# Performance work log

Measured on AMD Instinct MI355X. Metric: run time of the kernel, lower is better.

Reference implementation:

```python
import jax, jax.numpy as jnp
import numpy as np

HEADS = 8
DIM_HEAD = 64
SCALE = DIM_HEAD ** -0.5


def setup_inputs() -> dict:
    key = jax.random.key(0)
    ks = jax.random.split(key, 6)
    b, n, t, d, cond_dim, hidden = 2, 8, 1024, 512, 512, HEADS * DIM_HEAD
    return {
        "x": jax.random.normal(ks[0], (b * n, t, d), dtype=jnp.float32),
        "label_emb_mm": jax.random.normal(ks[1], (b, n, cond_dim), dtype=jnp.float32),
        "Wqkv": jax.random.normal(ks[2], (d, 3 * hidden), dtype=jnp.float32) * (d ** -0.5),
        "Wk": jax.random.normal(ks[3], (cond_dim, hidden), dtype=jnp.float32) * (cond_dim ** -0.5),
        "Wv": jax.random.normal(ks[4], (cond_dim, hidden), dtype=jnp.float32) * (cond_dim ** -0.5),
        "Wout": jax.random.normal(ks[5], (hidden, d), dtype=jnp.float32) * (hidden ** -0.5),
        "b": 2,
    }


def reference(x, label_emb_mm, Wqkv, Wk, Wv, Wout, b):
    bn, t, d = x.shape
    n = bn // b
    h, dh = HEADS, DIM_HEAD
    xb = x.reshape(b, n, t, d)
    # fused QKV projection: (b, n, t, 3*h*dh)
    qkv = xb @ Wqkv
    q, k, v = jnp.split(qkv, 3, axis=-1)

    def to_heads(z):  # (b, n, t, h*dh) -> (b, n, h, t, dh)
        return z.reshape(b, n, t, h, dh).transpose(0, 1, 3, 2, 4)

    q, k, v = to_heads(q), to_heads(k), to_heads(v)
    # per-frame conditioning K/V: one extra token per frame
    ek = (label_emb_mm @ Wk).reshape(b, n, 1, h, dh).transpose(0, 1, 3, 2, 4)
    ev = (label_emb_mm @ Wv).reshape(b, n, 1, h, dh).transpose(0, 1, 3, 2, 4)
    k = jnp.concatenate([ek, k], axis=-2)  # (b, n, h, 1+t, dh)
    v = jnp.concatenate([ev, v], axis=-2)
    q = q * SCALE
    sim = jnp.einsum("bnhid,bnhjd->bnhij", q, k)
    attn = jax.nn.softmax(sim, axis=-1)
    out = jnp.einsum("bnhij,bnhjd->bnhid", attn, v)
    out = out.transpose(0, 1, 3, 2, 4).reshape(b, n, t, h * dh)
    out = out @ Wout
    return out.reshape(b * n, t, d)
```

## Files before the change

kernel.cpp:

```cpp
#include <hip/hip_runtime.h>
#include <stdint.h>

typedef unsigned short u16;
typedef __bf16 bf16x8 __attribute__((ext_vector_type(8)));
typedef float f32x4 __attribute__((ext_vector_type(4)));
typedef float f32x16 __attribute__((ext_vector_type(16)));

__device__ __forceinline__ u16 f2bf(float f) {
  uint32_t u = __builtin_bit_cast(uint32_t, f);
  u += 0x7FFFu + ((u >> 16) & 1u);
  return (u16)(u >> 16);
}
__device__ __forceinline__ float bf2f(u16 v) {
  return __builtin_bit_cast(float, ((uint32_t)v) << 16);
}

#if __has_builtin(__builtin_amdgcn_exp2f)
__device__ __forceinline__ float exp2_fast(float x) { return __builtin_amdgcn_exp2f(x); }
#else
__device__ __forceinline__ float exp2_fast(float x) { return exp2f(x); }
#endif

__device__ __forceinline__ void gload_lds16(const u16* g, u16* l) {
  __builtin_amdgcn_global_load_lds(
      (const __attribute__((address_space(1))) uint32_t*)g,
      (__attribute__((address_space(3))) uint32_t*)l, 16, 0, 0);
}

__device__ __forceinline__ uint32_t cvtpk(float lo, float hi) {
  uint32_t r;
  asm("v_cvt_pk_bf16_f32 %0, %1, %2" : "=v"(r) : "v"(lo), "v"(hi));
  return r;
}
__device__ __forceinline__ void plswap(uint32_t& a, uint32_t& b) {
  asm volatile("v_permlane32_swap_b32 %0, %1" : "+v"(a), "+v"(b));
}

__global__ __launch_bounds__(256) void prep_kernel(
    const float* __restrict__ x, const float* __restrict__ Wqkv,
    const float* __restrict__ Wout, const float* __restrict__ label,
    const float* __restrict__ Wk, const float* __restrict__ Wv,
    u16* __restrict__ xb, u16* __restrict__ WqkvT, u16* __restrict__ WoutT,
    u16* __restrict__ ek, u16* __restrict__ ev, float qscale) {
  const int b = blockIdx.x;
  if (b < 4096) {
    int i = (b * 256 + threadIdx.x) * 8;
    float4 a = *(const float4*)(x + i);
    float4 c = *(const float4*)(x + i + 4);
    union { u16 u[8]; uint4 v; } r;
    r.u[0] = f2bf(a.x); r.u[1] = f2bf(a.y); r.u[2] = f2bf(a.z); r.u[3] = f2bf(a.w);
    r.u[4] = f2bf(c.x); r.u[5] = f2bf(c.y); r.u[6] = f2bf(c.z); r.u[7] = f2bf(c.w);
    *(uint4*)(xb + i) = r.v;
  } else if (b < 7168) {
    int id = (b - 4096) * 256 + threadIdx.x;
    int k = id & 511, nn = id >> 9;
    float v = Wqkv[(size_t)k * 1536 + nn];
    if (nn < 512) v *= qscale;
    WqkvT[id] = f2bf(v);
  } else if (b < 8192) {
    int id = (b - 7168) * 256 + threadIdx.x;
    int k = id & 511, nn = id >> 9;
    WoutT[id] = f2bf(Wout[(size_t)k * 512 + nn]);
  } else {
    __shared__ float sdata[256];
    const int bb = b - 8192;
    const int chunk = bb & 7, row = (bb >> 3) & 15;
    const float* W = (bb & 128) ? Wv : Wk;
    u16* o = (bb & 128) ? ev : ek;
    const int tid = threadIdx.x;
    const int col = chunk * 64 + (tid & 63);
    const int ks = tid >> 6;
    const float* lr = label + row * 512 + ks * 128;
    const float* wp = W + (size_t)(ks * 128) * 512 + col;
    float acc = 0.f;
#pragma unroll 8
    for (int i = 0; i < 128; ++i)
      acc = fmaf(lr[i], wp[(size_t)i * 512], acc);
    sdata[tid] = acc;
    __syncthreads();
    if (tid < 64) {
      float t = sdata[tid] + sdata[tid + 64] + sdata[tid + 128] + sdata[tid + 192];
      o[row * 512 + chunk * 64 + tid] = f2bf(t);
    }
  }
}

template <int MODE>
__global__ __launch_bounds__(512, 2) void gemm_bt_kernel(
    const u16* __restrict__ A, const u16* __restrict__ B,
    u16* __restrict__ OQ, u16* __restrict__ OKb, u16* __restrict__ OVT,
    float* __restrict__ OF, int K, int N) {
  constexpr int BN = (MODE == 0) ? 192 : 128;
  constexpr int NI = BN / 64;
  constexpr int NRB = BN / 64;
  constexpr int NBY = (MODE == 0) ? 8 : 4;
  constexpr int VM = 4 + NRB;

  __shared__ __align__(16) u16 As[2][256 * 64];
  __shared__ __align__(16) u16 Bs[2][BN * 64];

  const int tid = threadIdx.x;
  const int w = tid >> 6, lane = tid & 63;
  const int l15 = lane & 15, lg = lane >> 4;
  const int wr = w >> 2, wc = w & 3;

  const int q8 = gridDim.x >> 3;
  const int wg = (blockIdx.x & 7) * q8 + (blockIdx.x >> 3);
  const int bx = wg / NBY, by = wg % NBY;

  const int srow = tid >> 3, schunk = tid & 7;
  const u16* Ag = A + (size_t)(bx * 256 + srow) * K + ((schunk ^ (srow & 7)) * 8);
  const u16* Bg = B + (size_t)(by * BN + srow) * K + ((schunk ^ (srow & 7)) * 8);

  int aoff[8][2], boff[NI][2];
#pragma unroll
  for (int mi = 0; mi < 8; ++mi)
#pragma unroll
    for (int ks = 0; ks < 2; ++ks) {
      const int row = wr * 128 + mi * 16 + l15;
      aoff[mi][ks] = row * 64 + (((ks * 4 + lg) ^ (row & 7)) * 8);
    }
#pragma unroll
  for (int ni = 0; ni < NI; ++ni)
#pragma unroll
    for (int ks = 0; ks < 2; ++ks) {
      const int row = wc * (BN / 4) + ni * 16 + l15;
      boff[ni][ks] = row * 64 + (((ks * 4 + lg) ^ (row & 7)) * 8);
    }

  f32x4 acc[8][NI] = {};

  const int nt = K >> 6;
#define STAGE(buf, k0)                                                       \
  {                                                                          \
    _Pragma("unroll") for (int ra = 0; ra < 4; ++ra)                         \
        gload_lds16(Ag + (k0) + (size_t)(ra * 64) * K,                       \
                    &As[buf][(ra * 64 + w * 8) * 64]);                       \
    _Pragma("unroll") for (int rb = 0; rb < NRB; ++rb)                       \
        gload_lds16(Bg + (k0) + (size_t)(rb * 64) * K,                       \
                    &Bs[buf][(rb * 64 + w * 8) * 64]);                       \
  }
#define COMPUTE(cb)                                                          \
  {                                                                          \
    const u16* Ab = &As[cb][0];                                              \
    const u16* Bb = &Bs[cb][0];                                              \
    _Pragma("unroll") for (int ks = 0; ks < 2; ++ks) {                       \
      bf16x8 a[8], b[NI];                                                    \
      _Pragma("unroll") for (int mi = 0; mi < 8; ++mi)                       \
          a[mi] = *(const bf16x8*)&Ab[aoff[mi][ks]];                         \
      _Pragma("unroll") for (int ni = 0; ni < NI; ++ni)                      \
          b[ni] = *(const bf16x8*)&Bb[boff[ni][ks]];                         \
      __builtin_amdgcn_s_setprio(1);                                         \
      _Pragma("unroll") for (int mi = 0; mi < 8; ++mi)                       \
          _Pragma("unroll") for (int ni = 0; ni < NI; ++ni)                  \
              acc[mi][ni] = __builtin_amdgcn_mfma_f32_16x16x32_bf16(          \
                  a[mi], b[ni], acc[mi][ni], 0, 0, 0);                       \
      __builtin_amdgcn_s_setprio(0);                                         \
    }                                                                        \
  }

  STAGE(0, 0);
  STAGE(1, 64);

  for (int t = 0; t < nt - 1; ++t) {
    if constexpr (VM == 7)
      asm volatile("s_waitcnt vmcnt(7)" ::: "memory");
    else
      asm volatile("s_waitcnt vmcnt(6)" ::: "memory");
    __builtin_amdgcn_s_barrier();
    __builtin_amdgcn_sched_barrier(0);
    COMPUTE(t & 1);
    if (t + 2 < nt) {
      __builtin_amdgcn_s_barrier();
      __builtin_amdgcn_sched_barrier(0);
      STAGE(t & 1, (t + 2) * 64);
    }
  }
  asm volatile("s_waitcnt vmcnt(0)" ::: "memory");
  __builtin_amdgcn_s_barrier();
  __builtin_amdgcn_sched_barrier(0);
  COMPUTE((nt - 1) & 1);
#undef STAGE
#undef COMPUTE

  const int row0 = bx * 256 + wr * 128 + lg * 4;
  if constexpr (MODE == 1) {
#pragma unroll
    for (int mi = 0; mi < 8; ++mi)
#pragma unroll
      for (int ni = 0; ni < NI; ++ni) {
        int col = by * BN + wc * (BN / 4) + ni * 16 + l15;
#pragma unroll
        for (int r = 0; r < 4; ++r)
          OF[(size_t)(row0 + mi * 16 + r) * N + col] = acc[mi][ni][r];
      }
  } else {
#pragma unroll
    for (int mi = 0; mi < 8; ++mi)
#pragma unroll
      for (int ni = 0; ni < NI; ++ni) {
        const int gcol = by * BN + wc * (BN / 4) + ni * 16 + l15;
        const int sect = gcol >> 9;
        const int colL = gcol & 511;
        if (sect < 2) {
          u16* O = sect ? OKb : OQ;
#pragma unroll
          for (int r = 0; r < 4; ++r)
            O[(size_t)(row0 + mi * 16 + r) * 512 + colL] = f2bf(acc[mi][ni][r]);
        } else {
          int h = colL >> 6, dh = colL & 63;
          int rr = row0 + mi * 16;
          int bn = rr >> 10, t0 = rr & 1023;
          ushort4 pk;
          pk.x = f2bf(acc[mi][ni][0]);
          pk.y = f2bf(acc[mi][ni][1]);
          pk.z = f2bf(acc[mi][ni][2]);
          pk.w = f2bf(acc[mi][ni][3]);
          *(ushort4*)&OVT[(size_t)((bn * 8 + h) * 64 + dh) * 1024 + t0] = pk;
        }
      }
  }
}

__global__ __launch_bounds__(256, 2) void attn_kernel(
    const u16* __restrict__ Qb, const u16* __restrict__ Kb, const u16* __restrict__ VTb,
    const u16* __restrict__ ekb, const u16* __restrict__ evb, u16* __restrict__ Ob) {
  __shared__ __align__(16) u16 Kl[64 * 64];
  __shared__ __align__(16) u16 Vl[64 * 64];

  const int tid = threadIdx.x;
  const int w = tid >> 6, lane = tid & 63;
  const int l31 = lane & 31, hi = lane >> 5;
  const int lb = (blockIdx.x & 7) * 64 + (blockIdx.x >> 3);
  const int head = lb >> 2, qt = lb & 3;
  const int bn = head >> 3, h = head & 7;
  const int q0 = qt * 256 + w * 64;

  const int sr = tid >> 3, sj = tid & 7;
  const int sdst = (sj ^ (sr & 7)) * 8;
  const u16* KgA = Kb + (size_t)(bn * 1024 + sr) * 512 + h * 64 + sj * 8;
  const u16* VgA = VTb + (size_t)(head * 64 + sr) * 1024 + sj * 8;
  u16* KlD = &Kl[sr * 64 + sdst];
  u16* VlD = &Vl[sr * 64 + sdst];

  uint4 kp0, kp1, vp0, vp1;
  {
    kp0 = *(const uint4*)(KgA);
    kp1 = *(const uint4*)(KgA + (size_t)32 * 512);
    vp0 = *(const uint4*)(VgA);
    vp1 = *(const uint4*)(VgA + (size_t)32 * 1024);
  }

  bf16x8 qf[2][4];
#pragma unroll
  for (int qs = 0; qs < 2; ++qs)
#pragma unroll
    for (int c = 0; c < 4; ++c)
      qf[qs][c] = *(const bf16x8*)(Qb + (size_t)(bn * 1024 + q0 + qs * 32 + l31) * 512 +
                                   h * 64 + c * 16 + hi * 8);

  bf16x8 bones1;
  {
    union { u16 u[8]; bf16x8 v; } ob;
#pragma unroll
    for (int j = 0; j < 8; ++j) ob.u[j] = (u16)0x3F80;
    bones1 = ob.v;
  }

  f32x16 acc[2][2];
  f32x16 acc5[2];
  {
    float dot[2] = {0.f, 0.f};
#pragma unroll
    for (int c = 0; c < 4; ++c) {
      bf16x8 ekf = *(const bf16x8*)(ekb + bn * 512 + h * 64 + c * 16 + hi * 8);
#pragma unroll
      for (int qs = 0; qs < 2; ++qs)
#pragma unroll
        for (int j = 0; j < 8; ++j)
          dot[qs] += (float)qf[qs][c][j] * (float)ekf[j];
    }
    union { u16 u[8]; bf16x8 v; } pef[2], evf[2];
#pragma unroll
    for (int qs = 0; qs < 2; ++qs) {
      uint32_t a = __builtin_bit_cast(uint32_t, dot[qs]), b = a;
      plswap(a, b);
      float part = (lane < 32) ? __builtin_bit_cast(float, b) : __builtin_bit_cast(float, a);
      float pe = exp2_fast(dot[qs] + part);
#pragma unroll
      for (int j = 0; j < 8; ++j) pef[qs].u[j] = 0;
      if (hi == 0) pef[qs].u[0] = f2bf(pe);
    }
#pragma unroll
    for (int dt = 0; dt < 2; ++dt) {
#pragma unroll
      for (int j = 0; j < 8; ++j) evf[dt].u[j] = 0;
      if (hi == 0) evf[dt].u[0] = evb[bn * 512 + h * 64 + dt * 32 + l31];
    }
    f32x16 z = {};
#pragma unroll
    for (int qs = 0; qs < 2; ++qs) {
#pragma unroll
      for (int dt = 0; dt < 2; ++dt)
        acc[qs][dt] = __builtin_amdgcn_mfma_f32_32x32x16_bf16(pef[qs].v, evf[dt].v, z, 0, 0, 0);
      acc5[qs] = __builtin_amdgcn_mfma_f32_32x32x16_bf16(pef[qs].v, bones1, z, 0, 0, 0);
    }
  }

  for (int jt = 0; jt < 16; ++jt) {
    __syncthreads();
    *(uint4*)(KlD) = kp0;
    *(uint4*)(KlD + 32 * 64) = kp1;
    *(uint4*)(VlD) = vp0;
    *(uint4*)(VlD + 32 * 64) = vp1;
    __syncthreads();

    if (jt < 15) {
      const int j0 = (jt + 1) * 64;
      kp0 = *(const uint4*)(KgA + (size_t)j0 * 512);
      kp1 = *(const uint4*)(KgA + (size_t)(j0 + 32) * 512);
      vp0 = *(const uint4*)(VgA + j0);
      vp1 = *(const uint4*)(VgA + j0 + (size_t)32 * 1024);
    }

#pragma unroll
    for (int sub = 0; sub < 2; ++sub) {
      const int rk = sub * 32 + l31;
      bf16x8 kb[4];
#pragma unroll
      for (int c = 0; c < 4; ++c)
        kb[c] = *(const bf16x8*)&Kl[rk * 64 + (((c * 2 + hi) ^ (rk & 7)) * 8)];

      f32x16 s[2] = {};
#pragma unroll
      for (int qs = 0; qs < 2; ++qs)
#pragma unroll
        for (int c = 0; c < 4; ++c)
          s[qs] = __builtin_amdgcn_mfma_f32_32x32x16_bf16(kb[c], qf[qs][c], s[qs], 0, 0, 0);

      bf16x8 pa[2][2];
#pragma unroll
      for (int qs = 0; qs < 2; ++qs) {
        uint32_t wd[8];
#pragma unroll
        for (int i = 0; i < 8; ++i)
          wd[i] = cvtpk(exp2_fast(s[qs][2 * i]), exp2_fast(s[qs][2 * i + 1]));
        plswap(wd[0], wd[2]);
        plswap(wd[1], wd[3]);
        plswap(wd[4], wd[6]);
        plswap(wd[5], wd[7]);
        union { uint32_t w[4]; bf16x8 v; } f0, f1;
        f0.w[0] = wd[0]; f0.w[1] = wd[1]; f0.w[2] = wd[2]; f0.w[3] = wd[3];
        f1.w[0] = wd[4]; f1.w[1] = wd[5]; f1.w[2] = wd[6]; f1.w[3] = wd[7];
        pa[qs][0] = f0.v;
        pa[qs][1] = f1.v;
      }

#pragma unroll
      for (int dt = 0; dt < 2; ++dt) {
        const int rv = dt * 32 + l31;
#pragma unroll
        for (int ch = 0; ch < 2; ++ch) {
          bf16x8 vb = *(const bf16x8*)&Vl[rv * 64 + (((sub * 4 + ch * 2 + hi) ^ (rv & 7)) * 8)];
#pragma unroll
          for (int qs = 0; qs < 2; ++qs)
            acc[qs][dt] = __builtin_amdgcn_mfma_f32_32x32x16_bf16(pa[qs][ch], vb, acc[qs][dt], 0, 0, 0);
        }
      }
#pragma unroll
      for (int qs = 0; qs < 2; ++qs)
#pragma unroll
        for (int ch = 0; ch < 2; ++ch)
          acc5[qs] = __builtin_amdgcn_mfma_f32_32x32x16_bf16(pa[qs][ch], bones1, acc5[qs], 0, 0, 0);
    }
  }

#pragma unroll
  for (int qs = 0; qs < 2; ++qs)
#pragma unroll
    for (int r = 0; r < 16; ++r) {
      const float inv = 1.0f / acc5[qs][r];
      const int q = q0 + qs * 32 + (r & 3) + 8 * (r >> 2) + 4 * hi;
      u16* op = Ob + (size_t)(bn * 1024 + q) * 512 + h * 64 + l31;
      op[0] = f2bf(acc[qs][0][r] * inv);
      op[32] = f2bf(acc[qs][1][r] * inv);
    }
}

extern "C" void kernel_launch(void* const* d_in, const int* in_sizes, int n_in,
                              void* d_out, int out_size, void* d_ws, size_t ws_size,
                              hipStream_t stream) {
  (void)in_sizes; (void)n_in; (void)out_size; (void)ws_size;
  const float* x     = (const float*)d_in[0];
  const float* label = (const float*)d_in[1];
  const float* Wqkv  = (const float*)d_in[2];
  const float* Wk    = (const float*)d_in[3];
  const float* Wv    = (const float*)d_in[4];
  const float* Wout  = (const float*)d_in[5];
  float* out = (float*)d_out;

  char* ws = (char*)d_ws;
  u16* xb    = (u16*)(ws);
  u16* WqkvT = (u16*)(ws + 16777216);
  u16* WoutT = (u16*)(ws + 18350080);
  u16* ekb   = (u16*)(ws + 18874368);
  u16* evb   = (u16*)(ws + 18890752);
  u16* Qbuf  = (u16*)(ws + 18907136);
  u16* Kbuf  = (u16*)(ws + 35684352);
  u16* VTbuf = (u16*)(ws + 52461568);

  const float qscale = 0.125f * 1.4426950408889634f;

  prep_kernel<<<8448, 256, 0, stream>>>(x, Wqkv, Wout, label, Wk, Wv,
                                        xb, WqkvT, WoutT, ekb, evb, qscale);

  gemm_bt_kernel<0><<<512, 512, 0, stream>>>(xb, WqkvT, Qbuf, Kbuf, VTbuf, nullptr, 512, 1536);

  attn_kernel<<<512, 256, 0, stream>>>(Qbuf, Kbuf, VTbuf, ekb, evb, xb);

  gemm_bt_kernel<1><<<256, 512, 0, stream>>>(xb, WoutT, nullptr, nullptr, nullptr, out, 512, 512);
}
```

Baseline: 120.2 us.

## Halve per-wave query rows in attention, double blocks, use direct global-to-LDS loads

The attention kernel now gives each wave 32 query rows instead of 64. It launches twice as many blocks (1024) and raises the launch-bounds occupancy hint from 2 to 4. K/V tiles are loaded straight into LDS with global_load_lds per wave, replacing the register-staged prefetch of the next tile. The aim is to cut register pressure and raise occupancy so more waves hide latency. In exchange, each K/V tile is reused by fewer queries, so K/V traffic per query doubles, and the register prefetch overlap is lost, leaving the load exposed between barriers.

Result: slower. 123.1 us (+2.4%).

```diff
diff --git a/kernel.cpp b/kernel.cpp
--- a/kernel.cpp
+++ b/kernel.cpp
@@ -222,7 +222,7 @@
   }
 }
 
-__global__ __launch_bounds__(256, 2) void attn_kernel(
+__global__ __launch_bounds__(256, 4) void attn_kernel(
     const u16* __restrict__ Qb, const u16* __restrict__ Kb, const u16* __restrict__ VTb,
     const u16* __restrict__ ekb, const u16* __restrict__ evb, u16* __restrict__ Ob) {
   __shared__ __align__(16) u16 Kl[64 * 64];
@@ -231,33 +231,23 @@
   const int tid = threadIdx.x;
   const int w = tid >> 6, lane = tid & 63;
   const int l31 = lane & 31, hi = lane >> 5;
-  const int lb = (blockIdx.x & 7) * 64 + (blockIdx.x >> 3);
-  const int head = lb >> 2, qt = lb & 3;
+  const int lb = (blockIdx.x & 7) * 128 + (blockIdx.x >> 3);
+  const int head = lb >> 3, qt = lb & 7;
   const int bn = head >> 3, h = head & 7;
-  const int q0 = qt * 256 + w * 64;
-
-  const int sr = tid >> 3, sj = tid & 7;
-  const int sdst = (sj ^ (sr & 7)) * 8;
-  const u16* KgA = Kb + (size_t)(bn * 1024 + sr) * 512 + h * 64 + sj * 8;
-  const u16* VgA = VTb + (size_t)(head * 64 + sr) * 1024 + sj * 8;
-  u16* KlD = &Kl[sr * 64 + sdst];
-  u16* VlD = &Vl[sr * 64 + sdst];
-
-  uint4 kp0, kp1, vp0, vp1;
-  {
-    kp0 = *(const uint4*)(KgA);
-    kp1 = *(const uint4*)(KgA + (size_t)32 * 512);
-    vp0 = *(const uint4*)(VgA);
-    vp1 = *(const uint4*)(VgA + (size_t)32 * 1024);
-  }
-
-  bf16x8 qf[2][4];
-#pragma unroll
-  for (int qs = 0; qs < 2; ++qs)
-#pragma unroll
-    for (int c = 0; c < 4; ++c)
-      qf[qs][c] = *(const bf16x8*)(Qb + (size_t)(bn * 1024 + q0 + qs * 32 + l31) * 512 +
-                                   h * 64 + c * 16 + hi * 8);
+  const int q0 = qt * 128 + w * 32;
+
+  const int srow = lane >> 3;
+  const int schunk = (lane & 7) ^ srow;
+  const u16* Kg0 = Kb + (size_t)(bn * 1024 + w * 16 + srow) * 512 + h * 64 + schunk * 8;
+  const u16* Vg0 = VTb + (size_t)(head * 64 + w * 16 + srow) * 1024 + schunk * 8;
+  u16* KlDst = &Kl[w * 1024];
+  u16* VlDst = &Vl[w * 1024];
+
+  bf16x8 qf[4];
+#pragma unroll
+  for (int c = 0; c < 4; ++c)
+    qf[c] = *(const bf16x8*)(Qb + (size_t)(bn * 1024 + q0 + l31) * 512 +
+                             h * 64 + c * 16 + hi * 8);
 
   bf16x8 bones1;
   {
@@ -267,30 +257,26 @@
     bones1 = ob.v;
   }
 
-  f32x16 acc[2][2];
-  f32x16 acc5[2];
+  f32x16 acc[2];
+  f32x16 acc5;
   {
-    float dot[2] = {0.f, 0.f};
+    float dot = 0.f;
 #pragma unroll
     for (int c = 0; c < 4; ++c) {
       bf16x8 ekf = *(const bf16x8*)(ekb + bn * 512 + h * 64 + c * 16 + hi * 8);
 #pragma unroll
-      for (int qs = 0; qs < 2; ++qs)
-#pragma unroll
-        for (int j = 0; j < 8; ++j)
-          dot[qs] += (float)qf[qs][c][j] * (float)ekf[j];
-    }
-    union { u16 u[8]; bf16x8 v; } pef[2], evf[2];
-#pragma unroll
-    for (int qs = 0; qs < 2; ++qs) {
-      uint32_t a = __builtin_bit_cast(uint32_t, dot[qs]), b = a;
-      plswap(a, b);
-      float part = (lane < 32) ? __builtin_bit_cast(float, b) : __builtin_bit_cast(float, a);
-      float pe = exp2_fast(dot[qs] + part);
-#pragma unroll
-      for (int j = 0; j < 8; ++j) pef[qs].u[j] = 0;
-      if (hi == 0) pef[qs].u[0] = f2bf(pe);
-    }
+      for (int j = 0; j < 8; ++j)
+        dot += (float)qf[c][j] * (float)ekf[j];
+    }
+    uint32_t a = __builtin_bit_cast(uint32_t, dot), b = a;
+    plswap(a, b);
+    float part = (lane < 32) ? __builtin_bit_cast(float, b) : __builtin_bit_cast(float, a);
+    float pe = exp2_fast(dot + part);
+
+    union { u16 u[8]; bf16x8 v; } pef, evf[2];
+#pragma unroll
+    for (int j = 0; j < 8; ++j) pef.u[j] = 0;
+    if (hi == 0) pef.u[0] = f2bf(pe);
 #pragma unroll
     for (int dt = 0; dt < 2; ++dt) {
 #pragma unroll
@@ -299,29 +285,19 @@
     }
     f32x16 z = {};
 #pragma unroll
-    for (int qs = 0; qs < 2; ++qs) {
-#pragma unroll
-      for (int dt = 0; dt < 2; ++dt)
-        acc[qs][dt] = __builtin_amdgcn_mfma_f32_32x32x16_bf16(pef[qs].v, evf[dt].v, z, 0, 0, 0);
-      acc5[qs] = __builtin_amdgcn_mfma_f32_32x32x16_bf16(pef[qs].v, bones1, z, 0, 0, 0);
-    }
+    for (int dt = 0; dt < 2; ++dt)
+      acc[dt] = __builtin_amdgcn_mfma_f32_32x32x16_bf16(pef.v, evf[dt].v, z, 0, 0, 0);
+    acc5 = __builtin_amdgcn_mfma_f32_32x32x16_bf16(pef.v, bones1, z, 0, 0, 0);
   }
 
   for (int jt = 0; jt < 16; ++jt) {
+    const int j0 = jt * 64;
     __syncthreads();
-    *(uint4*)(KlD) = kp0;
-    *(uint4*)(KlD + 32 * 64) = kp1;
-    *(uint4*)(VlD) = vp0;
-    *(uint4*)(VlD + 32 * 64) = vp1;
+    gload_lds16(Kg0 + (size_t)j0 * 512, KlDst);
+    gload_lds16(Kg0 + (size_t)(j0 + 8) * 512, KlDst + 512);
+    gload_lds16(Vg0 + j0, VlDst);
+    gload_lds16(Vg0 + j0 + (size_t)8 * 1024, VlDst + 512);
     __syncthreads();
-
-    if (jt < 15) {
-      const int j0 = (jt + 1) * 64;
-      kp0 = *(const uint4*)(KgA + (size_t)j0 * 512);
-      kp1 = *(const uint4*)(KgA + (size_t)(j0 + 32) * 512);
-      vp0 = *(const uint4*)(VgA + j0);
-      vp1 = *(const uint4*)(VgA + j0 + (size_t)32 * 1024);
-    }
 
 #pragma unroll
     for (int sub = 0; sub < 2; ++sub) {
@@ -331,60 +307,45 @@
       for (int c = 0; c < 4; ++c)
         kb[c] = *(const bf16x8*)&Kl[rk * 64 + (((c * 2 + hi) ^ (rk & 7)) * 8)];
 
-      f32x16 s[2] = {};
-#pragma unroll
-      for (int qs = 0; qs < 2; ++qs)
-#pragma unroll
-        for (int c = 0; c < 4; ++c)
-          s[qs] = __builtin_amdgcn_mfma_f32_32x32x16_bf16(kb[c], qf[qs][c], s[qs], 0, 0, 0);
-
-      bf16x8 pa[2][2];
-#pragma unroll
-      for (int qs = 0; qs < 2; ++qs) {
-        uint32_t wd[8];
-#pragma unroll
-        for (int i = 0; i < 8; ++i)
-          wd[i] = cvtpk(exp2_fast(s[qs][2 * i]), exp2_fast(s[qs][2 * i + 1]));
-        plswap(wd[0], wd[2]);
-        plswap(wd[1], wd[3]);
-        plswap(wd[4], wd[6]);
-        plswap(wd[5], wd[7]);
-        union { uint32_t w[4]; bf16x8 v; } f0, f1;
-        f0.w[0] = wd[0]; f0.w[1] = wd[1]; f0.w[2] = wd[2]; f0.w[3] = wd[3];
-        f1.w[0] = wd[4]; f1.w[1] = wd[5]; f1.w[2] = wd[6]; f1.w[3] = wd[7];
-        pa[qs][0] = f0.v;
-        pa[qs][1] = f1.v;
-      }
+      f32x16 s = {};
+#pragma unroll
+      for (int c = 0; c < 4; ++c)
+        s = __builtin_amdgcn_mfma_f32_32x32x16_bf16(kb[c], qf[c], s, 0, 0, 0);
+
+      uint32_t wd[8];
+#pragma unroll
+      for (int i = 0; i < 8; ++i)
+        wd[i] = cvtpk(exp2_fast(s[2 * i]), exp2_fast(s[2 * i + 1]));
+      plswap(wd[0], wd[2]);
+      plswap(wd[1], wd[3]);
+      plswap(wd[4], wd[6]);
+      plswap(wd[5], wd[7]);
+      union { uint32_t w[4]; bf16x8 v; } f0, f1;
+      f0.w[0] = wd[0]; f0.w[1] = wd[1]; f0.w[2] = wd[2]; f0.w[3] = wd[3];
+      f1.w[0] = wd[4]; f1.w[1] = wd[5]; f1.w[2] = wd[6]; f1.w[3] = wd[7];
+      bf16x8 pa0 = f0.v, pa1 = f1.v;
 
 #pragma unroll
       for (int dt = 0; dt < 2; ++dt) {
         const int rv = dt * 32 + l31;
-#pragma unroll
-        for (int ch = 0; ch < 2; ++ch) {
-          bf16x8 vb = *(const bf16x8*)&Vl[rv * 64 + (((sub * 4 + ch * 2 + hi) ^ (rv & 7)) * 8)];
-#pragma unroll
-          for (int qs = 0; qs < 2; ++qs)
-            acc[qs][dt] = __builtin_amdgcn_mfma_f32_32x32x16_bf16(pa[qs][ch], vb, acc[qs][dt], 0, 0, 0);
-        }
+        bf16x8 vb0 = *(const bf16x8*)&Vl[rv * 64 + (((sub * 4 + hi) ^ (rv & 7)) * 8)];
+        acc[dt] = __builtin_amdgcn_mfma_f32_32x32x16_bf16(pa0, vb0, acc[dt], 0, 0, 0);
+        bf16x8 vb1 = *(const bf16x8*)&Vl[rv * 64 + (((sub * 4 + 2 + hi) ^ (rv & 7)) * 8)];
+        acc[dt] = __builtin_amdgcn_mfma_f32_32x32x16_bf16(pa1, vb1, acc[dt], 0, 0, 0);
       }
-#pragma unroll
-      for (int qs = 0; qs < 2; ++qs)
-#pragma unroll
-        for (int ch = 0; ch < 2; ++ch)
-          acc5[qs] = __builtin_amdgcn_mfma_f32_32x32x16_bf16(pa[qs][ch], bones1, acc5[qs], 0, 0, 0);
-    }
-  }
-
-#pragma unroll
-  for (int qs = 0; qs < 2; ++qs)
-#pragma unroll
-    for (int r = 0; r < 16; ++r) {
-      const float inv = 1.0f / acc5[qs][r];
-      const int q = q0 + qs * 32 + (r & 3) + 8 * (r >> 2) + 4 * hi;
-      u16* op = Ob + (size_t)(bn * 1024 + q) * 512 + h * 64 + l31;
-      op[0] = f2bf(acc[qs][0][r] * inv);
-      op[32] = f2bf(acc[qs][1][r] * inv);
-    }
+      acc5 = __builtin_amdgcn_mfma_f32_32x32x16_bf16(pa0, bones1, acc5, 0, 0, 0);
+      acc5 = __builtin_amdgcn_mfma_f32_32x32x16_bf16(pa1, bones1, acc5, 0, 0, 0);
+    }
+  }
+
+#pragma unroll
+  for (int r = 0; r < 16; ++r) {
+    const float inv = 1.0f / acc5[r];
+    const int q = q0 + (r & 3) + 8 * (r >> 2) + 4 * hi;
+    u16* op = Ob + (size_t)(bn * 1024 + q) * 512 + h * 64 + l31;
+    op[0] = f2bf(acc[0][r] * inv);
+    op[32] = f2bf(acc[1][r] * inv);
+  }
 }
 
 extern "C" void kernel_launch(void* const* d_in, const int* in_sizes, int n_in,
@@ -416,7 +377,7 @@
 
   gemm_bt_kernel<0><<<512, 512, 0, stream>>>(xb, WqkvT, Qbuf, Kbuf, VTbuf, nullptr, 512, 1536);
 
-  attn_kernel<<<512, 256, 0, stream>>>(Qbuf, Kbuf, VTbuf, ekb, evb, xb);
+  attn_kernel<<<1024, 256, 0, stream>>>(Qbuf, Kbuf, VTbuf, ekb, evb, xb);
 
   gemm_bt_kernel<1><<<256, 512, 0, stream>>>(xb, WoutT, nullptr, nullptr, nullptr, out, 512, 512);
 }
```

## Shrink GEMM tiles to 128 rows with 4-wave blocks and more workgroups

Applied to the files above, without the earlier changes.

Both projection GEMMs move from 256-row tiles with 8 waves per block to 128-row tiles with 4 waves per block, doubling the grid size. The warp-to-subtile mapping, LDS staging and wait counts are reworked to match. The aim is better CU occupancy and load balance on a device with many CUs, since the old grids of 512 and 256 blocks underfill it. The cost is less operand reuse per block and more global and LDS traffic per FLOP.

After: 116.7 us (median of 2 runs). -2.9%, faster.

```diff
diff --git a/kernel.cpp b/kernel.cpp
--- a/kernel.cpp
+++ b/kernel.cpp
@@ -86,87 +86,90 @@
 }
 
 template <int MODE>
-__global__ __launch_bounds__(512, 2) void gemm_bt_kernel(
+__global__ __launch_bounds__(256, 2) void gemm_bt_kernel(
     const u16* __restrict__ A, const u16* __restrict__ B,
     u16* __restrict__ OQ, u16* __restrict__ OKb, u16* __restrict__ OVT,
     float* __restrict__ OF, int K, int N) {
   constexpr int BN = (MODE == 0) ? 192 : 128;
-  constexpr int NI = BN / 64;
-  constexpr int NRB = BN / 64;
+  constexpr int NA = (MODE == 0) ? 8 : 4;
+  constexpr int NB = (MODE == 0) ? 3 : 4;
+  constexpr int A_ISS = 4;
+  constexpr int B_ISS = BN / 32;
   constexpr int NBY = (MODE == 0) ? 8 : 4;
-  constexpr int VM = 4 + NRB;
-
-  __shared__ __align__(16) u16 As[2][256 * 64];
+
+  __shared__ __align__(16) u16 As[2][128 * 64];
   __shared__ __align__(16) u16 Bs[2][BN * 64];
 
   const int tid = threadIdx.x;
   const int w = tid >> 6, lane = tid & 63;
   const int l15 = lane & 15, lg = lane >> 4;
-  const int wr = w >> 2, wc = w & 3;
 
   const int q8 = gridDim.x >> 3;
   const int wg = (blockIdx.x & 7) * q8 + (blockIdx.x >> 3);
   const int bx = wg / NBY, by = wg % NBY;
 
-  const int srow = tid >> 3, schunk = tid & 7;
-  const u16* Ag = A + (size_t)(bx * 256 + srow) * K + ((schunk ^ (srow & 7)) * 8);
-  const u16* Bg = B + (size_t)(by * BN + srow) * K + ((schunk ^ (srow & 7)) * 8);
-
-  int aoff[8][2], boff[NI][2];
-#pragma unroll
-  for (int mi = 0; mi < 8; ++mi)
+  const int srow = lane >> 3;
+  const int schunk = (lane & 7) ^ srow;
+  const u16* Ag = A + (size_t)(bx * 128 + srow) * K + schunk * 8;
+  const u16* Bg = B + (size_t)(by * BN + srow) * K + schunk * 8;
+
+  int aoff[NA][2], boff[NB][2];
+#pragma unroll
+  for (int mi = 0; mi < NA; ++mi)
 #pragma unroll
     for (int ks = 0; ks < 2; ++ks) {
-      const int row = wr * 128 + mi * 16 + l15;
+      const int row = ((MODE == 0) ? 0 : (w >> 1) * 64) + mi * 16 + l15;
       aoff[mi][ks] = row * 64 + (((ks * 4 + lg) ^ (row & 7)) * 8);
     }
 #pragma unroll
-  for (int ni = 0; ni < NI; ++ni)
+  for (int ni = 0; ni < NB; ++ni)
 #pragma unroll
     for (int ks = 0; ks < 2; ++ks) {
-      const int row = wc * (BN / 4) + ni * 16 + l15;
+      const int row = ((MODE == 0) ? w * 48 : (w & 1) * 64) + ni * 16 + l15;
       boff[ni][ks] = row * 64 + (((ks * 4 + lg) ^ (row & 7)) * 8);
     }
 
-  f32x4 acc[8][NI] = {};
+  f32x4 acc[NA][NB] = {};
 
   const int nt = K >> 6;
-#define STAGE(buf, k0)                                                       \
-  {                                                                          \
-    _Pragma("unroll") for (int ra = 0; ra < 4; ++ra)                         \
-        gload_lds16(Ag + (k0) + (size_t)(ra * 64) * K,                       \
-                    &As[buf][(ra * 64 + w * 8) * 64]);                       \
-    _Pragma("unroll") for (int rb = 0; rb < NRB; ++rb)                       \
-        gload_lds16(Bg + (k0) + (size_t)(rb * 64) * K,                       \
-                    &Bs[buf][(rb * 64 + w * 8) * 64]);                       \
-  }
-#define COMPUTE(cb)                                                          \
-  {                                                                          \
-    const u16* Ab = &As[cb][0];                                              \
-    const u16* Bb = &Bs[cb][0];                                              \
-    _Pragma("unroll") for (int ks = 0; ks < 2; ++ks) {                       \
-      bf16x8 a[8], b[NI];                                                    \
-      _Pragma("unroll") for (int mi = 0; mi < 8; ++mi)                       \
-          a[mi] = *(const bf16x8*)&Ab[aoff[mi][ks]];                         \
-      _Pragma("unroll") for (int ni = 0; ni < NI; ++ni)                      \
-          b[ni] = *(const bf16x8*)&Bb[boff[ni][ks]];                         \
-      __builtin_amdgcn_s_setprio(1);                                         \
-      _Pragma("unroll") for (int mi = 0; mi < 8; ++mi)                       \
-          _Pragma("unroll") for (int ni = 0; ni < NI; ++ni)                  \
-              acc[mi][ni] = __builtin_amdgcn_mfma_f32_16x16x32_bf16(          \
-                  a[mi], b[ni], acc[mi][ni], 0, 0, 0);                       \
-      __builtin_amdgcn_s_setprio(0);                                         \
-    }                                                                        \
+#define STAGE(buf, k0)                                                        \
+  {                                                                           \
+    _Pragma("unroll") for (int i = 0; i < A_ISS; ++i) {                       \
+      const int j = i * 4 + w;                                                \
+      gload_lds16(Ag + (k0) + (size_t)(j * 8) * K, &As[buf][(j * 8) * 64]);   \
+    }                                                                         \
+    _Pragma("unroll") for (int i = 0; i < B_ISS; ++i) {                       \
+      const int j = i * 4 + w;                                                \
+      gload_lds16(Bg + (k0) + (size_t)(j * 8) * K, &Bs[buf][(j * 8) * 64]);   \
+    }                                                                         \
+  }
+#define COMPUTE(cb)                                                           \
+  {                                                                           \
+    const u16* Ab = &As[cb][0];                                               \
+    const u16* Bb = &Bs[cb][0];                                               \
+    _Pragma("unroll") for (int ks = 0; ks < 2; ++ks) {                        \
+      bf16x8 a[NA], b[NB];                                                    \
+      _Pragma("unroll") for (int mi = 0; mi < NA; ++mi)                       \
+          a[mi] = *(const bf16x8*)&Ab[aoff[mi][ks]];                          \
+      _Pragma("unroll") for (int ni = 0; ni < NB; ++ni)                       \
+          b[ni] = *(const bf16x8*)&Bb[boff[ni][ks]];                          \
+      __builtin_amdgcn_s_setprio(1);                                          \
+      _Pragma("unroll") for (int mi = 0; mi < NA; ++mi)                       \
+          _Pragma("unroll") for (int ni = 0; ni < NB; ++ni)                   \
+              acc[mi][ni] = __builtin_amdgcn_mfma_f32_16x16x32_bf16(           \
+                  a[mi], b[ni], acc[mi][ni], 0, 0, 0);                        \
+      __builtin_amdgcn_s_setprio(0);                                          \
+    }                                                                         \
   }
 
   STAGE(0, 0);
   STAGE(1, 64);
 
   for (int t = 0; t < nt - 1; ++t) {
-    if constexpr (VM == 7)
-      asm volatile("s_waitcnt vmcnt(7)" ::: "memory");
+    if constexpr (A_ISS + B_ISS == 10)
+      asm volatile("s_waitcnt vmcnt(10)" ::: "memory");
     else
-      asm volatile("s_waitcnt vmcnt(6)" ::: "memory");
+      asm volatile("s_waitcnt vmcnt(8)" ::: "memory");
     __builtin_amdgcn_s_barrier();
     __builtin_amdgcn_sched_barrier(0);
     COMPUTE(t & 1);
@@ -183,23 +186,24 @@
 #undef STAGE
 #undef COMPUTE
 
-  const int row0 = bx * 256 + wr * 128 + lg * 4;
   if constexpr (MODE == 1) {
-#pragma unroll
-    for (int mi = 0; mi < 8; ++mi)
-#pragma unroll
-      for (int ni = 0; ni < NI; ++ni) {
-        int col = by * BN + wc * (BN / 4) + ni * 16 + l15;
+    const int row0 = bx * 128 + (w >> 1) * 64 + lg * 4;
+#pragma unroll
+    for (int mi = 0; mi < NA; ++mi)
+#pragma unroll
+      for (int ni = 0; ni < NB; ++ni) {
+        int col = by * BN + (w & 1) * 64 + ni * 16 + l15;
 #pragma unroll
         for (int r = 0; r < 4; ++r)
           OF[(size_t)(row0 + mi * 16 + r) * N + col] = acc[mi][ni][r];
       }
   } else {
-#pragma unroll
-    for (int mi = 0; mi < 8; ++mi)
-#pragma unroll
-      for (int ni = 0; ni < NI; ++ni) {
-        const int gcol = by * BN + wc * (BN / 4) + ni * 16 + l15;
+    const int row0 = bx * 128 + lg * 4;
+#pragma unroll
+    for (int mi = 0; mi < NA; ++mi)
+#pragma unroll
+      for (int ni = 0; ni < NB; ++ni) {
+        const int gcol = by * BN + w * 48 + ni * 16 + l15;
         const int sect = gcol >> 9;
         const int colL = gcol & 511;
         if (sect < 2) {
@@ -414,9 +418,9 @@
   prep_kernel<<<8448, 256, 0, stream>>>(x, Wqkv, Wout, label, Wk, Wv,
                                         xb, WqkvT, WoutT, ekb, evb, qscale);
 
-  gemm_bt_kernel<0><<<512, 512, 0, stream>>>(xb, WqkvT, Qbuf, Kbuf, VTbuf, nullptr, 512, 1536);
+  gemm_bt_kernel<0><<<1024, 256, 0, stream>>>(xb, WqkvT, Qbuf, Kbuf, VTbuf, nullptr, 512, 1536);
 
   attn_kernel<<<512, 256, 0, stream>>>(Qbuf, Kbuf, VTbuf, ekb, evb, xb);
 
-  gemm_bt_kernel<1><<<256, 512, 0, stream>>>(xb, WoutT, nullptr, nullptr, nullptr, out, 512, 512);
-}
+  gemm_bt_kernel<1><<<512, 256, 0, stream>>>(xb, WoutT, nullptr, nullptr, nullptr, out, 512, 512);
+}
```
